# Kernel optimization log

Measured on AMD Instinct MI355X. Metric: run time of the kernel, lower is better.

The kernel has to match this reference:

```python
import jax, jax.numpy as jnp
import numpy as np

B, L, D, H = 4, 1024, 1024, 16
DH = D // H
NEG = -1e9


def setup_inputs() -> dict:
    key = jax.random.key(0)
    ks = jax.random.split(key, 8)
    sequence = jax.random.normal(ks[0], (B, L, D), dtype=jnp.float32)
    # additive padding mask: all tokens valid -> zeros
    padding_mask = jnp.zeros((B, 1, 1, L), dtype=jnp.float32)
    # additive causal dependency mask: -1e9 above the diagonal
    causal = jnp.triu(jnp.full((L, L), NEG, dtype=jnp.float32), k=1)
    dependency_mask = causal[None, None, :, :]
    scale = 1.0 / np.sqrt(D)
    Wq = jax.random.normal(ks[1], (D, D), dtype=jnp.float32) * scale
    Wk = jax.random.normal(ks[2], (D, D), dtype=jnp.float32) * scale
    Wv = jax.random.normal(ks[3], (D, D), dtype=jnp.float32) * scale
    bq = jnp.zeros((D,), dtype=jnp.float32)
    bk = jnp.zeros((D,), dtype=jnp.float32)
    bv = jnp.zeros((D,), dtype=jnp.float32)
    return {"sequence": sequence, "padding_mask": padding_mask,
            "dependency_mask": dependency_mask,
            "Wq": Wq, "bq": bq, "Wk": Wk, "bk": bk, "Wv": Wv, "bv": bv}


def reference(sequence, padding_mask, dependency_mask, Wq, bq, Wk, bk, Wv, bv):
    b, l, d = sequence.shape
    h, dh = H, d // H
    # Q/K/V linear projections (torch Linear: x @ W^T + b)
    q = (sequence @ Wq.T + bq).reshape(b, l, h, dh)
    k = (sequence @ Wk.T + bk).reshape(b, l, h, dh)
    v = (sequence @ Wv.T + bv).reshape(b, l, h, dh)
    # scaled dot-product scores: [B, H, L, L]
    scores = jnp.einsum('blhd,bmhd->bhlm', q, k) / jnp.sqrt(jnp.float32(dh))
    scores = scores + padding_mask + dependency_mask
    attn = jax.nn.softmax(scores, axis=-1)
    # dropout is identity in eval mode (training=False)
    out = jnp.einsum('bhlm,bmhd->blhd', attn, v)
    return out.reshape(b, l, d)
```

## Files before the change

kernel.cpp:

```cpp
#include <hip/hip_runtime.h>
#include <hip/hip_bf16.h>


#define LL 1024

typedef __attribute__((ext_vector_type(8))) short short8;
typedef __attribute__((ext_vector_type(4))) float floatx4;

__device__ __forceinline__ float bf2f(unsigned short u) {
    return __uint_as_float(((unsigned int)u) << 16);
}
__device__ __forceinline__ unsigned short f2bf(float f) {
    unsigned int x = __float_as_uint(f);
    unsigned int r = x + 0x7fffu + ((x >> 16) & 1u);
    return (unsigned short)(r >> 16);
}

#if __has_builtin(__builtin_amdgcn_global_load_lds)
#define HAVE_GLL 1
typedef __attribute__((address_space(1))) unsigned int as1_u32;
typedef __attribute__((address_space(3))) unsigned int as3_u32;
__device__ __forceinline__ void gll16(const void* g, void* l) {
    __builtin_amdgcn_global_load_lds((const as1_u32*)g, (as3_u32*)l, 16, 0, 0);
}
#endif

#if __has_builtin(__builtin_amdgcn_exp2f)
#define EXP2F(x) __builtin_amdgcn_exp2f(x)
#else
#define EXP2F(x) exp2f(x)
#endif

__global__ __launch_bounds__(256) void conv_in(
    const float* __restrict__ seq, const float* __restrict__ wq,
    const float* __restrict__ wk,  const float* __restrict__ wv,
    const float* __restrict__ bq,  const float* __restrict__ bk,
    const float* __restrict__ bv,  const float* __restrict__ pm,
    unsigned short* __restrict__ ws)
{
    unsigned int t = blockIdx.x * 256u + threadIdx.x;
    if (t >= 918400u) return;
    unsigned int e = t * 8u;
    const float* src; unsigned int idx; unsigned short* dst; float scale = 1.0f;
    if (e < 4194304u)      { src = seq; idx = e;            dst = ws + 12582912u; }
    else if (e < 5242880u) { src = wq;  idx = e - 4194304u; dst = ws + 16777216u; }
    else if (e < 6291456u) { src = wk;  idx = e - 5242880u; dst = ws + 17825792u; }
    else if (e < 7340032u) { src = wv;  idx = e - 6291456u; dst = ws + 18874368u; }
    else if (e < 7341056u) { src = bq;  idx = e - 7340032u; dst = ws + 20971520u; }
    else if (e < 7342080u) { src = bk;  idx = e - 7341056u; dst = ws + 20972544u; }
    else if (e < 7343104u) { src = bv;  idx = e - 7342080u; dst = ws + 20973568u; }
    else { src = pm; idx = e - 7343104u; dst = ws + 20974592u; scale = 1.4426950f; }
    float4 a = *(const float4*)(src + idx);
    float4 c = *(const float4*)(src + idx + 4);
    uint4 st;
    st.x = (unsigned)f2bf(a.x * scale) | ((unsigned)f2bf(a.y * scale) << 16);
    st.y = (unsigned)f2bf(a.z * scale) | ((unsigned)f2bf(a.w * scale) << 16);
    st.z = (unsigned)f2bf(c.x * scale) | ((unsigned)f2bf(c.y * scale) << 16);
    st.w = (unsigned)f2bf(c.z * scale) | ((unsigned)f2bf(c.w * scale) << 16);
    *(uint4*)(dst + idx) = st;
}

__global__ __launch_bounds__(256) void qkv_proj(
    const unsigned short* __restrict__ X,
    const unsigned short* __restrict__ Wq, const unsigned short* __restrict__ bq,
    const unsigned short* __restrict__ Wk, const unsigned short* __restrict__ bk,
    const unsigned short* __restrict__ Wv, const unsigned short* __restrict__ bv,
    unsigned short* __restrict__ dst_base)
{
    const int z = blockIdx.z;
    const unsigned short* W    = (z == 0) ? Wq : ((z == 1) ? Wk : Wv);
    const unsigned short* bias = (z == 0) ? bq : ((z == 1) ? bk : bv);
    const float osc = (z == 0) ? 0.18033688f : 1.0f;
    unsigned short* dst = dst_base + (size_t)z * (4096u * 1024u);

    __shared__ __align__(16) unsigned short AsF[8192];
    __shared__ __align__(16) unsigned short BsF[8192];

    const int tid  = threadIdx.x;
    const int lane = tid & 63;
    const int wave = tid >> 6;
    const int quad = lane >> 4, r16 = lane & 15;
    const int wr = wave >> 1, wc = wave & 1;
    const int m0 = blockIdx.x * 128;
    const int n0 = blockIdx.y * 128;

    const int st_r3  = lane >> 3;
    const int st_col = ((lane & 7) ^ st_r3) << 3;

    floatx4 acc[4][4];
#pragma unroll
    for (int i = 0; i < 4; ++i)
#pragma unroll
        for (int j = 0; j < 4; ++j)
#pragma unroll
            for (int r = 0; r < 4; ++r) acc[i][j][r] = 0.f;

    for (int k0 = 0; k0 < 1024; k0 += 64) {
        __syncthreads();
#ifdef HAVE_GLL
#pragma unroll
        for (int c2 = 0; c2 < 4; ++c2) {
            int seg = wave * 4 + c2;
            int row = seg * 8 + st_r3;
            gll16(X + (size_t)(m0 + row) * 1024 + k0 + st_col, &AsF[seg * 512]);
            gll16(W + (size_t)(n0 + row) * 1024 + k0 + st_col, &BsF[seg * 512]);
        }
#else
#pragma unroll
        for (int c2 = 0; c2 < 4; ++c2) {
            int seg = wave * 4 + c2;
            int row = seg * 8 + st_r3;
            *(uint4*)&AsF[seg * 512 + lane * 8] = *(const uint4*)(X + (size_t)(m0 + row) * 1024 + k0 + st_col);
            *(uint4*)&BsF[seg * 512 + lane * 8] = *(const uint4*)(W + (size_t)(n0 + row) * 1024 + k0 + st_col);
        }
#endif
        __syncthreads();

#pragma unroll
        for (int kk = 0; kk < 2; ++kk) {
            const int csw = ((kk * 4 + quad) ^ (r16 & 7)) << 3;
            short8 a[4], b[4];
#pragma unroll
            for (int i = 0; i < 4; ++i)
                a[i] = *(const short8*)&AsF[(wr * 64 + i * 16 + r16) * 64 + csw];
#pragma unroll
            for (int j = 0; j < 4; ++j)
                b[j] = *(const short8*)&BsF[(wc * 64 + j * 16 + r16) * 64 + csw];
#pragma unroll
            for (int i = 0; i < 4; ++i)
#pragma unroll
                for (int j = 0; j < 4; ++j)
                    acc[i][j] = __builtin_amdgcn_mfma_f32_16x16x32_bf16(a[i], b[j], acc[i][j], 0, 0, 0);
        }
    }

#pragma unroll
    for (int j = 0; j < 4; ++j) {
        int n = n0 + wc * 64 + j * 16 + r16;
        float bvf = bf2f(bias[n]);
        int h = n >> 6, d = n & 63;
#pragma unroll
        for (int i = 0; i < 4; ++i) {
            int m_base = m0 + wr * 64 + i * 16 + quad * 4;
            int b = m_base >> 10, l0 = m_base & 1023;
            if (z == 2) {
                ushort4 st;
                st.x = f2bf(acc[i][j][0] + bvf); st.y = f2bf(acc[i][j][1] + bvf);
                st.z = f2bf(acc[i][j][2] + bvf); st.w = f2bf(acc[i][j][3] + bvf);
                *(ushort4*)&dst[(((size_t)(b * 16 + h)) * 64 + d) * 1024 + l0] = st;
            } else {
#pragma unroll
                for (int r = 0; r < 4; ++r)
                    dst[(((size_t)(b * 16 + h)) * 1024 + (l0 + r)) * 64 + d] =
                        f2bf((acc[i][j][r] + bvf) * osc);
            }
        }
    }
}

__global__ __launch_bounds__(256) void attn(
    const unsigned short* __restrict__ Qw,
    const unsigned short* __restrict__ Kw,
    const unsigned short* __restrict__ Vt_g,
    const unsigned short* __restrict__ pmask,
    float* __restrict__ out)
{
    __shared__ __align__(16) unsigned short KsF[8192];
    __shared__ __align__(16) unsigned short VsF[8192];
    __shared__ __align__(16) unsigned short PsF[2][4][2048];

    const int tid  = threadIdx.x;
    const int lane = tid & 63;
    const int wave = tid >> 6;
    const int quad = lane >> 4, r16 = lane & 15;

    const int bid  = blockIdx.x;
    const int half = bid >> 8, idx = bid & 255;
    const int bh   = idx & 63;
    const int qb   = idx >> 6;
    const int qi   = half ? (7 - qb) : qb;
    const int b    = bh >> 4, h = bh & 15;
    const int q0   = qi << 7;

    const size_t base = (size_t)bh * (1024 * 64);
    const unsigned short* Qg = Qw + base;
    const unsigned short* Kg = Kw + base;
    const unsigned short* Vg = Vt_g + base;

    const int kst_r3  = lane >> 3;
    const int kst_col = ((lane & 7) ^ kst_r3) << 3;
    const int vst_r   = lane >> 4;

    short8 aq[2][2];
#pragma unroll
    for (int f = 0; f < 2; ++f) {
        int qrow = q0 + f * 64 + wave * 16 + r16;
        aq[f][0] = *(const short8*)(Qg + (size_t)qrow * 64 + quad * 8);
        aq[f][1] = *(const short8*)(Qg + (size_t)qrow * 64 + 32 + quad * 8);
    }

    short8 ones;
#pragma unroll
    for (int i = 0; i < 8; ++i) ones[i] = (short)0x3f80;

    floatx4 ol[2];
    floatx4 o[2][4];
#pragma unroll
    for (int f = 0; f < 2; ++f)
#pragma unroll
        for (int r = 0; r < 4; ++r) ol[f][r] = 0.f;
#pragma unroll
    for (int f = 0; f < 2; ++f)
#pragma unroll
        for (int j = 0; j < 4; ++j)
#pragma unroll
            for (int r = 0; r < 4; ++r) o[f][j][r] = 0.f;

    for (int kt = 0; kt <= qi; ++kt) {
        float pm2[8];
#pragma unroll
        for (int j = 0; j < 8; ++j)
            pm2[j] = bf2f(pmask[b * LL + kt * 128 + j * 16 + r16]) - 12.0f;

        __syncthreads();
#ifdef HAVE_GLL
#pragma unroll
        for (int c2 = 0; c2 < 4; ++c2) {
            int seg = wave * 4 + c2;
            int krow = seg * 8 + kst_r3;
            gll16(Kg + (size_t)(kt * 128 + krow) * 64 + kst_col, &KsF[seg * 512]);
            int vrow = seg * 4 + vst_r;
            int vcol = (((lane & 15) ^ (vrow & 7))) << 3;
            gll16(Vg + (size_t)vrow * 1024 + kt * 128 + vcol, &VsF[seg * 512]);
        }
#else
#pragma unroll
        for (int c2 = 0; c2 < 4; ++c2) {
            int seg = wave * 4 + c2;
            int krow = seg * 8 + kst_r3;
            *(uint4*)&KsF[seg * 512 + lane * 8] =
                *(const uint4*)(Kg + (size_t)(kt * 128 + krow) * 64 + kst_col);
            int vrow = seg * 4 + vst_r;
            int vcol = (((lane & 15) ^ (vrow & 7))) << 3;
            *(uint4*)&VsF[seg * 512 + lane * 8] =
                *(const uint4*)(Vg + (size_t)vrow * 1024 + kt * 128 + vcol);
        }
#endif
        __syncthreads();

#pragma unroll
        for (int f = 0; f < 2; ++f) {
            floatx4 s[8];
#pragma unroll
            for (int j = 0; j < 8; ++j)
#pragma unroll
                for (int r = 0; r < 4; ++r) s[j][r] = 0.f;
#pragma unroll
            for (int j = 0; j < 8; ++j) {
                short8 bk0 = *(const short8*)&KsF[(j * 16 + r16) * 64 + (((0 * 4 + quad) ^ (r16 & 7)) << 3)];
                s[j] = __builtin_amdgcn_mfma_f32_16x16x32_bf16(aq[f][0], bk0, s[j], 0, 0, 0);
                short8 bk1 = *(const short8*)&KsF[(j * 16 + r16) * 64 + (((1 * 4 + quad) ^ (r16 & 7)) << 3)];
                s[j] = __builtin_amdgcn_mfma_f32_16x16x32_bf16(aq[f][1], bk1, s[j], 0, 0, 0);
            }

            if (kt == qi) {
                const int my_q = q0 + f * 64 + wave * 16 + quad * 4;
#pragma unroll
                for (int j = 0; j < 8; ++j) {
                    int key = kt * 128 + j * 16 + r16;
#pragma unroll
                    for (int r = 0; r < 4; ++r)
                        if (key > my_q + r) s[j][r] -= 1.0e9f;
                }
            }

#pragma unroll
            for (int j = 0; j < 8; ++j) {
                int key = j * 16 + r16;
                int ab = ((key >> 5) << 9) + (((key >> 3) & 3) << 7) + (key & 7) + (quad << 5);
#pragma unroll
                for (int r = 0; r < 4; ++r) {
                    float p = EXP2F(s[j][r] + pm2[j]);
                    PsF[f][wave][ab + (r << 3)] = (unsigned short)(__float_as_uint(p) >> 16);
                }
            }
            asm volatile("s_waitcnt lgkmcnt(0)" ::: "memory");

#pragma unroll
            for (int kk4 = 0; kk4 < 4; ++kk4) {
                short8 ap = *(const short8*)&PsF[f][wave][kk4 * 512 + lane * 8];
                ol[f] = __builtin_amdgcn_mfma_f32_16x16x32_bf16(ap, ones, ol[f], 0, 0, 0);
#pragma unroll
                for (int j2 = 0; j2 < 4; ++j2) {
                    short8 bv = *(const short8*)&VsF[(j2 * 16 + r16) * 128 + (((kk4 * 4 + quad) ^ (r16 & 7)) << 3)];
                    o[f][j2] = __builtin_amdgcn_mfma_f32_16x16x32_bf16(ap, bv, o[f][j2], 0, 0, 0);
                }
            }
        }
    }

#pragma unroll
    for (int f = 0; f < 2; ++f) {
        float linv[4];
#pragma unroll
        for (int r = 0; r < 4; ++r)
            linv[r] = 1.0f / fmaxf(ol[f][r], 1.0e-30f);
        const int my_q = q0 + f * 64 + wave * 16 + quad * 4;
#pragma unroll
        for (int j2 = 0; j2 < 4; ++j2) {
            int d = j2 * 16 + r16;
#pragma unroll
            for (int r = 0; r < 4; ++r) {
                size_t oidx = ((size_t)(b * 1024 + my_q + r)) * 1024 + h * 64 + d;
                out[oidx] = o[f][j2][r] * linv[r];
            }
        }
    }
}

__global__ __launch_bounds__(256) void fill_sentinel_f(float* __restrict__ out,
                                                       float v, unsigned int n)
{
    unsigned int t = blockIdx.x * 256u + threadIdx.x;
    if (t < n) out[t] = v;
}

extern "C" void kernel_launch(void* const* d_in, const int* in_sizes, int n_in,
                              void* d_out, int out_size, void* d_ws, size_t ws_size,
                              hipStream_t stream) {
    bool sizes_ok = (n_in == 9) && in_sizes[0] == 4194304 && in_sizes[1] == 4096 &&
                    in_sizes[2] == 1048576 && in_sizes[3] == 1048576 && in_sizes[4] == 1024 &&
                    in_sizes[5] == 1048576 && in_sizes[6] == 1024 && in_sizes[7] == 1048576 &&
                    in_sizes[8] == 1024 && out_size == 4194304;
    if (!sizes_ok) {
        fill_sentinel_f<<<16384, 256, 0, stream>>>((float*)d_out, 100.0f, 4194304u);
        return;
    }
    if (ws_size < 50331652u) {
        fill_sentinel_f<<<16384, 256, 0, stream>>>((float*)d_out, 200.0f, 4194304u);
        return;
    }

    unsigned short* ws = (unsigned short*)d_ws;

    conv_in<<<3588, 256, 0, stream>>>(
        (const float*)d_in[0], (const float*)d_in[3], (const float*)d_in[5],
        (const float*)d_in[7], (const float*)d_in[4], (const float*)d_in[6],
        (const float*)d_in[8], (const float*)d_in[1], ws);

    const unsigned short* cseq = ws + 12582912u;
    const unsigned short* cwq  = ws + 16777216u;
    const unsigned short* cwk  = ws + 17825792u;
    const unsigned short* cwv  = ws + 18874368u;
    const unsigned short* cbq  = ws + 20971520u;
    const unsigned short* cbk  = ws + 20972544u;
    const unsigned short* cbv  = ws + 20973568u;
    const unsigned short* cpm  = ws + 20974592u;

    dim3 g1(32, 8, 3);
    qkv_proj<<<g1, 256, 0, stream>>>(cseq, cwq, cbq, cwk, cbk, cwv, cbv, ws);

    attn<<<512, 256, 0, stream>>>(ws, ws + 4194304u, ws + 8388608u, cpm, (float*)d_out);
}
```

Baseline: 158.1 us.

## Double-buffer QKV projection GEMM with 256x256 tiles and interleaved prefetch

Rewrites the QKV projection GEMM to use 256x256 output tiles with 512 threads (8 waves) and double-buffered LDS. Global-to-LDS loads for the next K step are issued between MFMA phases, and setprio raises wave priority around the MFMA bursts. The aim is to overlap memory traffic with matrix math and to raise reuse per tile. The cost is 128KB of LDS per block and a grid of only 192 blocks, which may leave the 256 CUs underfilled.

```diff
diff --git a/kernel.cpp b/kernel.cpp
--- a/kernel.cpp
+++ b/kernel.cpp
@@ -60,7 +60,7 @@
     *(uint4*)(dst + idx) = st;
 }
 
-__global__ __launch_bounds__(256) void qkv_proj(
+__global__ __launch_bounds__(512, 2) void qkv_proj(
     const unsigned short* __restrict__ X,
     const unsigned short* __restrict__ Wq, const unsigned short* __restrict__ bq,
     const unsigned short* __restrict__ Wk, const unsigned short* __restrict__ bk,
@@ -68,70 +68,154 @@
     unsigned short* __restrict__ dst_base)
 {
     const int z = blockIdx.z;
-    const unsigned short* W    = (z == 0) ? Wq : ((z == 1) ? Wk : Wv);
+    const unsigned short* Wm   = (z == 0) ? Wq : ((z == 1) ? Wk : Wv);
     const unsigned short* bias = (z == 0) ? bq : ((z == 1) ? bk : bv);
     const float osc = (z == 0) ? 0.18033688f : 1.0f;
     unsigned short* dst = dst_base + (size_t)z * (4096u * 1024u);
 
-    __shared__ __align__(16) unsigned short AsF[8192];
-    __shared__ __align__(16) unsigned short BsF[8192];
+    __shared__ __align__(16) unsigned short Abuf[2][16384];
+    __shared__ __align__(16) unsigned short Bbuf[2][16384];
 
     const int tid  = threadIdx.x;
     const int lane = tid & 63;
     const int wave = tid >> 6;
     const int quad = lane >> 4, r16 = lane & 15;
-    const int wr = wave >> 1, wc = wave & 1;
-    const int m0 = blockIdx.x * 128;
-    const int n0 = blockIdx.y * 128;
-
-    const int st_r3  = lane >> 3;
-    const int st_col = ((lane & 7) ^ st_r3) << 3;
-
-    floatx4 acc[4][4];
-#pragma unroll
-    for (int i = 0; i < 4; ++i)
+    const int wr = wave >> 2, wc = wave & 3;
+    const int m0 = blockIdx.x * 256;
+    const int n0 = blockIdx.y * 256;
+
+    const int r3   = lane >> 3;
+    const int stc  = ((lane & 7) ^ r3) << 3;
+    const int seg0 = wave * 4;
+
+    const unsigned short* Asrc = X  + (size_t)(m0 + seg0 * 8 + r3) * 1024 + stc;
+    const unsigned short* Bsrc = Wm + (size_t)(n0 + seg0 * 8 + r3) * 1024 + stc;
+
+    floatx4 acc[8][4];
+#pragma unroll
+    for (int i = 0; i < 8; ++i)
 #pragma unroll
         for (int j = 0; j < 4; ++j)
 #pragma unroll
             for (int r = 0; r < 4; ++r) acc[i][j][r] = 0.f;
 
-    for (int k0 = 0; k0 < 1024; k0 += 64) {
-        __syncthreads();
 #ifdef HAVE_GLL
 #pragma unroll
-        for (int c2 = 0; c2 < 4; ++c2) {
-            int seg = wave * 4 + c2;
-            int row = seg * 8 + st_r3;
-            gll16(X + (size_t)(m0 + row) * 1024 + k0 + st_col, &AsF[seg * 512]);
-            gll16(W + (size_t)(n0 + row) * 1024 + k0 + st_col, &BsF[seg * 512]);
-        }
+    for (int c = 0; c < 4; ++c) {
+        gll16(Asrc + (size_t)c * 8192, &Abuf[0][(seg0 + c) * 512]);
+        gll16(Bsrc + (size_t)c * 8192, &Bbuf[0][(seg0 + c) * 512]);
+    }
 #else
 #pragma unroll
-        for (int c2 = 0; c2 < 4; ++c2) {
-            int seg = wave * 4 + c2;
-            int row = seg * 8 + st_r3;
-            *(uint4*)&AsF[seg * 512 + lane * 8] = *(const uint4*)(X + (size_t)(m0 + row) * 1024 + k0 + st_col);
-            *(uint4*)&BsF[seg * 512 + lane * 8] = *(const uint4*)(W + (size_t)(n0 + row) * 1024 + k0 + st_col);
-        }
-#endif
-        __syncthreads();
-
-#pragma unroll
-        for (int kk = 0; kk < 2; ++kk) {
-            const int csw = ((kk * 4 + quad) ^ (r16 & 7)) << 3;
-            short8 a[4], b[4];
-#pragma unroll
-            for (int i = 0; i < 4; ++i)
-                a[i] = *(const short8*)&AsF[(wr * 64 + i * 16 + r16) * 64 + csw];
+    for (int c = 0; c < 4; ++c) {
+        *(uint4*)&Abuf[0][(seg0 + c) * 512 + lane * 8] = *(const uint4*)(Asrc + (size_t)c * 8192);
+        *(uint4*)&Bbuf[0][(seg0 + c) * 512 + lane * 8] = *(const uint4*)(Bsrc + (size_t)c * 8192);
+    }
+#endif
+    asm volatile("s_waitcnt vmcnt(0) lgkmcnt(0)" ::: "memory");
+    __builtin_amdgcn_s_barrier();
+
+#pragma unroll 2
+    for (int t = 0; t < 16; ++t) {
+        const int cur = t & 1;
+        const int nxt = cur ^ 1;
+        const int k0n = (t + 1) << 6;
+        const unsigned short* Ac = Abuf[cur];
+        const unsigned short* Bc = Bbuf[cur];
+        const int arow = (wr * 128 + r16) * 64;
+        const int brow = (wc * 64 + r16) * 64;
+        const int c0 = ((0 + quad) ^ (r16 & 7)) << 3;
+        const int c1 = ((4 + quad) ^ (r16 & 7)) << 3;
+        short8 a[4], b[4];
+
+#pragma unroll
+        for (int i = 0; i < 4; ++i)
+            a[i] = *(const short8*)&Ac[arow + i * 1024 + c0];
+#pragma unroll
+        for (int j = 0; j < 4; ++j)
+            b[j] = *(const short8*)&Bc[brow + j * 1024 + c0];
+        if (t < 15) {
+#ifdef HAVE_GLL
+#pragma unroll
+            for (int c = 0; c < 4; ++c)
+                gll16(Asrc + (size_t)c * 8192 + k0n, &Abuf[nxt][(seg0 + c) * 512]);
+#else
+#pragma unroll
+            for (int c = 0; c < 4; ++c)
+                *(uint4*)&Abuf[nxt][(seg0 + c) * 512 + lane * 8] =
+                    *(const uint4*)(Asrc + (size_t)c * 8192 + k0n);
+#endif
+        }
+        __builtin_amdgcn_s_barrier();
+        asm volatile("s_waitcnt lgkmcnt(0)" ::: "memory");
+        __builtin_amdgcn_s_setprio(1);
+#pragma unroll
+        for (int i = 0; i < 4; ++i)
 #pragma unroll
             for (int j = 0; j < 4; ++j)
-                b[j] = *(const short8*)&BsF[(wc * 64 + j * 16 + r16) * 64 + csw];
-#pragma unroll
-            for (int i = 0; i < 4; ++i)
-#pragma unroll
-                for (int j = 0; j < 4; ++j)
-                    acc[i][j] = __builtin_amdgcn_mfma_f32_16x16x32_bf16(a[i], b[j], acc[i][j], 0, 0, 0);
-        }
+                acc[i][j] = __builtin_amdgcn_mfma_f32_16x16x32_bf16(a[i], b[j], acc[i][j], 0, 0, 0);
+        __builtin_amdgcn_s_setprio(0);
+        __builtin_amdgcn_s_barrier();
+
+#pragma unroll
+        for (int i = 0; i < 4; ++i)
+            a[i] = *(const short8*)&Ac[arow + (4 + i) * 1024 + c0];
+        if (t < 15) {
+#ifdef HAVE_GLL
+#pragma unroll
+            for (int c = 0; c < 4; ++c)
+                gll16(Bsrc + (size_t)c * 8192 + k0n, &Bbuf[nxt][(seg0 + c) * 512]);
+#else
+#pragma unroll
+            for (int c = 0; c < 4; ++c)
+                *(uint4*)&Bbuf[nxt][(seg0 + c) * 512 + lane * 8] =
+                    *(const uint4*)(Bsrc + (size_t)c * 8192 + k0n);
+#endif
+        }
+        __builtin_amdgcn_s_barrier();
+        asm volatile("s_waitcnt lgkmcnt(0)" ::: "memory");
+        __builtin_amdgcn_s_setprio(1);
+#pragma unroll
+        for (int i = 0; i < 4; ++i)
+#pragma unroll
+            for (int j = 0; j < 4; ++j)
+                acc[4 + i][j] = __builtin_amdgcn_mfma_f32_16x16x32_bf16(a[i], b[j], acc[4 + i][j], 0, 0, 0);
+        __builtin_amdgcn_s_setprio(0);
+        __builtin_amdgcn_s_barrier();
+
+#pragma unroll
+        for (int i = 0; i < 4; ++i)
+            a[i] = *(const short8*)&Ac[arow + i * 1024 + c1];
+#pragma unroll
+        for (int j = 0; j < 4; ++j)
+            b[j] = *(const short8*)&Bc[brow + j * 1024 + c1];
+        __builtin_amdgcn_s_barrier();
+        asm volatile("s_waitcnt lgkmcnt(0)" ::: "memory");
+        __builtin_amdgcn_s_setprio(1);
+#pragma unroll
+        for (int i = 0; i < 4; ++i)
+#pragma unroll
+            for (int j = 0; j < 4; ++j)
+                acc[i][j] = __builtin_amdgcn_mfma_f32_16x16x32_bf16(a[i], b[j], acc[i][j], 0, 0, 0);
+        __builtin_amdgcn_s_setprio(0);
+        __builtin_amdgcn_s_barrier();
+
+#pragma unroll
+        for (int i = 0; i < 4; ++i)
+            a[i] = *(const short8*)&Ac[arow + (4 + i) * 1024 + c1];
+        __builtin_amdgcn_s_barrier();
+        asm volatile("s_waitcnt lgkmcnt(0)" ::: "memory");
+        __builtin_amdgcn_s_setprio(1);
+#pragma unroll
+        for (int i = 0; i < 4; ++i)
+#pragma unroll
+            for (int j = 0; j < 4; ++j)
+                acc[4 + i][j] = __builtin_amdgcn_mfma_f32_16x16x32_bf16(a[i], b[j], acc[4 + i][j], 0, 0, 0);
+        __builtin_amdgcn_s_setprio(0);
+        if (t < 15) {
+            asm volatile("s_waitcnt vmcnt(0) lgkmcnt(0)" ::: "memory");
+        }
+        __builtin_amdgcn_s_barrier();
     }
 
 #pragma unroll
@@ -140,8 +224,8 @@
         float bvf = bf2f(bias[n]);
         int h = n >> 6, d = n & 63;
 #pragma unroll
-        for (int i = 0; i < 4; ++i) {
-            int m_base = m0 + wr * 64 + i * 16 + quad * 4;
+        for (int i = 0; i < 8; ++i) {
+            int m_base = m0 + wr * 128 + i * 16 + quad * 4;
             int b = m_base >> 10, l0 = m_base & 1023;
             if (z == 2) {
                 ushort4 st;
@@ -357,8 +441,8 @@
     const unsigned short* cbv  = ws + 20973568u;
     const unsigned short* cpm  = ws + 20974592u;
 
-    dim3 g1(32, 8, 3);
-    qkv_proj<<<g1, 256, 0, stream>>>(cseq, cwq, cbq, cwk, cbk, cwv, cbv, ws);
+    dim3 g1(16, 4, 3);
+    qkv_proj<<<g1, 512, 0, stream>>>(cseq, cwq, cbq, cwk, cbk, cwv, cbv, ws);
 
     attn<<<512, 256, 0, stream>>>(ws, ws + 4194304u, ws + 8388608u, cpm, (float*)d_out);
 }
```

Result: no change. 157.0 us (-0.7%).
